# Kernel optimization log

Hardware: AMD Instinct MI355X
Metric: run time of the kernel (lower is better)

Reference implementation:

```python
import jax, jax.numpy as jnp
import numpy as np


def conv4d(x, w, b):
    """Valid 4D convolution.
    x: [B, Cin, T, D, H, W]; w: [Cout, Cin, kT, kD, kH, kW]; b: [Cout].
    Implemented as a fixed small loop over the kT kernel offsets, folding the
    output T positions into the batch of a 3D convolution (same math as the
    standard conv4d-via-conv3d decomposition used in torch).
    """
    B, Cin, T, D, H, W = x.shape
    Cout, _, kT, kD, kH, kW = w.shape
    To = T - kT + 1
    Do, Ho, Wo = D - kD + 1, H - kH + 1, W - kW + 1
    out = jnp.zeros((B * To, Cout, Do, Ho, Wo), dtype=x.dtype)
    for i in range(kT):  # kT in {3,4}: small fixed loop
        xs = jax.lax.slice_in_dim(x, i, i + To, axis=2)          # [B,Cin,To,D,H,W]
        xs = xs.transpose(0, 2, 1, 3, 4, 5).reshape(B * To, Cin, D, H, W)
        out = out + jax.lax.conv_general_dilated(
            xs, w[:, :, i], window_strides=(1, 1, 1), padding='VALID',
            dimension_numbers=('NCDHW', 'OIDHW', 'NCDHW'))
    out = out.reshape(B, To, Cout, Do, Ho, Wo).transpose(0, 2, 1, 3, 4, 5)
    return out + b[None, :, None, None, None, None]


def setup_inputs() -> dict:
    key = jax.random.key(0)
    ks = jax.random.split(key, 14)
    s = 0.1
    inp = {
        'x':  jax.random.normal(ks[0], (256, 1, 18, 18, 18, 18), dtype=jnp.float32),
        'w1': jax.random.normal(ks[1], (3, 1, 4, 4, 4, 4), dtype=jnp.float32) * s,
        'b1': jnp.zeros((3,), dtype=jnp.float32),
        'w2': jax.random.normal(ks[2], (3, 3, 4, 4, 4, 4), dtype=jnp.float32) * s,
        'b2': jnp.zeros((3,), dtype=jnp.float32),
        'w3': jax.random.normal(ks[3], (4, 3, 4, 4, 4, 4), dtype=jnp.float32) * s,
        'b3': jnp.zeros((4,), dtype=jnp.float32),
        'w4': jax.random.normal(ks[4], (5, 4, 4, 4, 4, 4), dtype=jnp.float32) * s,
        'b4': jnp.zeros((5,), dtype=jnp.float32),
        'w5': jax.random.normal(ks[5], (5, 5, 3, 3, 3, 3), dtype=jnp.float32) * s,
        'b5': jnp.zeros((5,), dtype=jnp.float32),
        'fc1_w': jax.random.normal(ks[6], (33, 1280), dtype=jnp.float32) * 0.02,
        'fc1_b': jnp.zeros((33,), dtype=jnp.float32),
        'fc2_w': jax.random.normal(ks[7], (1, 33), dtype=jnp.float32) * 0.02,
        'fc2_b': jnp.zeros((1,), dtype=jnp.float32),
    }
    return inp


def reference(x, w1, b1, w2, b2, w3, b3, w4, b4, w5, b5, fc1_w, fc1_b, fc2_w, fc2_b):
    h = jax.nn.relu(conv4d(x, w1, b1))
    h = jax.nn.relu(conv4d(h, w2, b2))
    h = jax.nn.relu(conv4d(h, w3, b3))
    h = jax.nn.relu(conv4d(h, w4, b4))
    h = jax.nn.relu(conv4d(h, w5, b5))   # [B, 5, 4, 4, 4, 4]
    h = h.reshape(h.shape[0], -1)        # [B, 1280]; Dropout is identity in eval
    h = jax.nn.relu(h @ fc1_w.T + fc1_b)
    return jax.nn.sigmoid(h @ fc2_w.T + fc2_b)  # [B, 1]
```

## Files before the change

kernel.cpp:

```cpp
#include <hip/hip_runtime.h>
#include <math.h>

#define BATCH 256
typedef unsigned int uint;
typedef unsigned short ushort;
typedef _Float16 half8 __attribute__((ext_vector_type(8)));
typedef float f32x4 __attribute__((ext_vector_type(4)));
typedef uint u32x4 __attribute__((ext_vector_type(4)));

#define GLOBAL_AS __attribute__((address_space(1)))
#define LDS_AS __attribute__((address_space(3)))

__device__ __forceinline__ ushort f2h(float f) {
  _Float16 h = (_Float16)f;
  return __builtin_bit_cast(ushort, h);
}
__device__ __forceinline__ float h2f(ushort u) {
  return (float)__builtin_bit_cast(_Float16, u);
}

template <int N>
__device__ __forceinline__ void waitv() {
  if constexpr (N == 0) {
    asm volatile("s_waitcnt vmcnt(0)" ::: "memory");
  } else if constexpr (N == 7) {
    asm volatile("s_waitcnt vmcnt(7)" ::: "memory");
  } else if constexpr (N == 9) {
    asm volatile("s_waitcnt vmcnt(9)" ::: "memory");
  } else if constexpr (N == 10) {
    asm volatile("s_waitcnt vmcnt(10)" ::: "memory");
  } else {
    static_assert(N == 0 || N == 7 || N == 9 || N == 10, "add literal");
  }
  __builtin_amdgcn_sched_barrier(0);
}

__global__ __launch_bounds__(256) void transpose_kernel(
    const float* __restrict__ x, uint* __restrict__ xt) {
  __shared__ uint tile[65][65];
  const int P = 104976, NPP = 52488;
  const int pp0 = blockIdx.x * 64, b0 = blockIdx.y * 64;
  const int tx = threadIdx.x & 63, ty = threadIdx.x >> 6;
  for (int r = 0; r < 64; r += 4) {
    const int bl = ty + r, pp = pp0 + tx;
    if (pp < NPP) {
      const float2 v = *(const float2*)(x + (size_t)(b0 + bl) * P + 2 * pp);
      tile[tx][bl] = (uint)f2h(v.x) | ((uint)f2h(v.y) << 16);
    }
  }
  if (threadIdx.x < 64 && pp0 + 64 < NPP) {
    const int bl = threadIdx.x;
    const float2 v =
        *(const float2*)(x + (size_t)(b0 + bl) * P + 2 * (pp0 + 64));
    tile[64][bl] = (uint)f2h(v.x) | ((uint)f2h(v.y) << 16);
  }
  __syncthreads();
  for (int r = ty; r < 64; r += 4) {
    const int pp = pp0 + r;
    if (pp >= NPP) break;
    const int wp = pp % 9, sh = pp / 9;
    if (wp & 1) continue;
    uint2 o;
    o.x = tile[r][tx];
    o.y = (wp == 8) ? 0u : tile[r + 1][tx];
    *(uint2*)(xt + (size_t)(sh * 5 + (wp >> 1)) * 512 + (b0 + tx) * 2) = o;
  }
}

template <int CIN, int COUT, int KK, int S>
__global__ __launch_bounds__(256) void build_b(
    const float* __restrict__ w, ushort* __restrict__ Bg) {
  const int chunk = blockIdx.x;
  const int kd = chunk % KK, kt = (chunk / KK) % KK, ci = chunk / (KK * KK);
  for (int e = threadIdx.x; e < 512; e += 256) {
    int n = e >> 5, k = e & 31;
    int kh = k >> 3, wi = k & 7;
    int co = n / S, dw = n % S;
    int kw = wi - dw;
    float v = 0.f;
    if (co < COUT && kh < KK && kw >= 0 && kw < KK)
      v = w[((((co * CIN + ci) * KK + kt) * KK + kd) * KK + kh) * KK + kw];
    Bg[chunk * 512 + n * 32 + k] = f2h(v);
  }
}

template <int CIN, int COUT, int KK, int TI, int GIN, int GOUT, int HB,
          int PADSTART, int PADEND>
__global__ __launch_bounds__(256) void conv_wave(
    const ushort* __restrict__ xin, const ushort* __restrict__ Bg,
    const float* __restrict__ bias, ushort* __restrict__ out) {
  constexpr int S = 4;
  constexpr int WO = TI - KK + 1;
  constexpr int HTILES = WO / HB;
  constexpr int NC = CIN * KK * KK;
  constexpr int RS = 4 + HB - 1;
  constexpr int CH = RS + 1;
  constexpr int sH = GIN * 1024, sD = TI * sH, sT = TI * sD, sC = TI * sT;
  constexpr int oH = GOUT * 1024, oD = WO * oH, oT = WO * oD, oC = WO * oT;

  __shared__ ushort slab[4][2][CH * 512];

  const int ht = blockIdx.x % HTILES;
  const int wt = blockIdx.x / HTILES;
  const int d = blockIdx.y, t = blockIdx.z;
  const int h0 = ht * HB, wb = wt * S;
  const int g0 = wb >> 2;

  const int tid = threadIdx.x;
  const int wave = tid >> 6, lane = tid & 63;
  const int quad = lane >> 4, mm = lane & 15;

  const int xsrc = (lane >> 5) * 1024 + wave * 256 + (lane & 31) * 8;
  const int bsrc = mm * 32 + quad * 8;

  f32x4 acc[HB][4];
#pragma unroll
  for (int dh = 0; dh < HB; dh++)
#pragma unroll
    for (int bt = 0; bt < 4; bt++) acc[dh][bt] = (f32x4){0.f, 0.f, 0.f, 0.f};

  auto stage = [&](int c, int buf) {
    const int kd = c % KK, kt2 = (c / KK) % KK, ci = c / (KK * KK);
    const ushort* base =
        xin + ci * sC + (t + kt2) * sT + (d + kd) * sD + h0 * sH + g0 * 1024;
    ushort* l = &slab[wave][buf][0];
#pragma unroll
    for (int r = 0; r < RS; r++)
      __builtin_amdgcn_global_load_lds(
          (const GLOBAL_AS uint*)(const void*)(base + r * sH + xsrc),
          (LDS_AS uint*)(void*)(l + r * 512), 16, 0, 0);
    __builtin_amdgcn_global_load_lds(
        (const GLOBAL_AS uint*)(const void*)(Bg + c * 512 + bsrc),
        (LDS_AS uint*)(void*)(l + RS * 512), 16, 0, 0);
  };

  stage(0, 0);

  for (int c = 0; c < NC; c++) {
    if (c + 1 < NC) {
      stage(c + 1, (c + 1) & 1);
      waitv<CH>();
    } else {
      waitv<0>();
    }
    const ushort* wsl = &slab[wave][c & 1][0];
    u32x4 traw = *(const u32x4*)(const void*)(wsl + RS * 512 + lane * 8);
    half8 tf = __builtin_bit_cast(half8, traw);
#pragma unroll
    for (int dh = 0; dh < HB; dh++) {
      const ushort* arow = wsl + (dh + quad) * 512;
#pragma unroll
      for (int bt = 0; bt < 4; bt++) {
        const int bb = bt * 16 + mm;
        uint2 lo = *(const uint2*)(const void*)(arow + bb * 4);
        uint2 hi = *(const uint2*)(const void*)(arow + 256 + bb * 4);
        half8 xf = __builtin_bit_cast(half8, (u32x4){lo.x, lo.y, hi.x, hi.y});
        acc[dh][bt] =
            __builtin_amdgcn_mfma_f32_16x16x32_f16(tf, xf, acc[dh][bt], 0, 0, 0);
      }
    }
  }

  const bool is_last = (wb + S >= WO);
  const int co = quad;
#pragma unroll
  for (int dh = 0; dh < HB; dh++)
#pragma unroll
    for (int bt = 0; bt < 4; bt++) {
      const int b = wave * 64 + bt * 16 + mm;
      ushort* obase = out + t * oT + d * oD + (h0 + dh) * oH + b * 4;
      f32x4 v = acc[dh][bt];
      if (co < COUT) {
        const float bv = bias[co];
        float r0 = (wb + 0 < WO) ? fmaxf(v[0] + bv, 0.f) : 0.f;
        float r1 = (wb + 1 < WO) ? fmaxf(v[1] + bv, 0.f) : 0.f;
        float r2 = (wb + 2 < WO) ? fmaxf(v[2] + bv, 0.f) : 0.f;
        float r3 = (wb + 3 < WO) ? fmaxf(v[3] + bv, 0.f) : 0.f;
        uint2 pk;
        pk.x = (uint)f2h(r0) | ((uint)f2h(r1) << 16);
        pk.y = (uint)f2h(r2) | ((uint)f2h(r3) << 16);
        *(uint2*)(void*)(obase + co * oC + g0 * 1024) = pk;
        if constexpr (PADEND > PADSTART) {
          if (is_last) {
#pragma unroll
            for (int w = PADSTART; w < PADEND; w += 2)
              *(uint*)(void*)(obase + co * oC + (w >> 2) * 1024 + (w & 3)) = 0u;
          }
        }
      }
    }
}

template <int CIN, int COUT, int KK, int TI, int GIN, int GOUT, int S, int HB,
          int PADSTART, int PADEND>
__global__ __launch_bounds__(256) void conv_mfma(
    const ushort* __restrict__ xin, const ushort* __restrict__ Bg,
    const float* __restrict__ bias, ushort* __restrict__ out) {
  constexpr int WO = TI - KK + 1;
  constexpr int HTILES = WO / HB;
  constexpr int NC = CIN * KK * KK;
  constexpr int RS = 4 + HB - 1;
  constexpr int GW = (S == 4 ? 2 : 3);
  constexpr int ROWU = GW * 1024;
  constexpr int PROW = GW * 2;
  constexpr int sH = GIN * 1024, sD = TI * sH, sT = TI * sD, sC = TI * sT;
  constexpr int oH = GOUT * 1024, oD = WO * oH, oT = WO * oD, oC = WO * oT;

  __shared__ ushort slab[2][RS * ROWU];

  const int ht = blockIdx.x % HTILES;
  const int wt = blockIdx.x / HTILES;
  const int d = blockIdx.y, t = blockIdx.z;
  const int h0 = ht * HB, wb = wt * S;
  const int g0 = wb >> 2;

  const int tid = threadIdx.x;
  const int wave = tid >> 6, lane = tid & 63;
  const int quad = lane >> 4, mm = lane & 15;

  f32x4 acc[HB][4];
#pragma unroll
  for (int dh = 0; dh < HB; dh++)
#pragma unroll
    for (int bt = 0; bt < 4; bt++) acc[dh][bt] = (f32x4){0.f, 0.f, 0.f, 0.f};

  auto stage = [&](int c, int buf) {
    const int kd = c % KK, kt2 = (c / KK) % KK, ci = c / (KK * KK);
    const ushort* base =
        xin + ci * sC + (t + kt2) * sT + (d + kd) * sD + g0 * 1024;
    for (int r = wave; r < RS; r += 4) {
      int row = h0 + r;
      if (row > TI - 1) row = TI - 1;
      const ushort* g = base + row * sH;
      ushort* l = &slab[buf][r * ROWU];
#pragma unroll
      for (int p = 0; p < PROW; p++) {
        __builtin_amdgcn_global_load_lds(
            (const GLOBAL_AS uint*)(const void*)(g + p * 512 + lane * 8),
            (LDS_AS uint*)(void*)(l + p * 512), 16, 0, 0);
      }
    }
  };

  stage(0, 0);

  for (int c = 0; c < NC; c++) {
    __syncthreads();
    if (c + 1 < NC) stage(c + 1, (c + 1) & 1);

    u32x4 traw = *(const u32x4*)(const void*)(Bg + c * 512 + mm * 32 + quad * 8);
    half8 tf = __builtin_bit_cast(half8, traw);
    const int buf = c & 1;

#pragma unroll
    for (int dh = 0; dh < HB; dh++) {
      const ushort* arow = &slab[buf][(dh + quad) * ROWU];
#pragma unroll
      for (int bt = 0; bt < 4; bt++) {
        const int bidx = ((wave * 4 + bt) * 16 + mm) * 4;
        u32x4 raw;
        if ((wb & 2) == 0) {
          uint2 lo = *(const uint2*)(const void*)(arow + bidx);
          uint2 hi = *(const uint2*)(const void*)(arow + 1024 + bidx);
          raw = (u32x4){lo.x, lo.y, hi.x, hi.y};
        } else {
          uint c0 = *(const uint*)(const void*)(arow + bidx + 2);
          uint2 md = *(const uint2*)(const void*)(arow + 1024 + bidx);
          uint c1 = *(const uint*)(const void*)(arow + 2048 + bidx);
          raw = (u32x4){c0, md.x, md.y, c1};
        }
        half8 xf = __builtin_bit_cast(half8, raw);
        acc[dh][bt] =
            __builtin_amdgcn_mfma_f32_16x16x32_f16(tf, xf, acc[dh][bt], 0, 0, 0);
      }
    }
  }

  const bool is_last = (wb + S >= WO);
#pragma unroll
  for (int dh = 0; dh < HB; dh++)
#pragma unroll
    for (int bt = 0; bt < 4; bt++) {
      const int b = (wave * 4 + bt) * 16 + mm;
      ushort* obase = out + t * oT + d * oD + (h0 + dh) * oH + b * 4;
      f32x4 v = acc[dh][bt];
      const int co0 = quad * 2, co1 = co0 + 1;
      if (co0 < COUT) {
        const float bv = bias[co0];
        float r0 = fmaxf(v[0] + bv, 0.f), r1 = fmaxf(v[1] + bv, 0.f);
        *(uint*)(void*)(obase + co0 * oC + g0 * 1024 + (wb & 3)) =
            (uint)f2h(r0) | ((uint)f2h(r1) << 16);
      }
      if (co1 < COUT) {
        const float bv = bias[co1];
        float r2 = fmaxf(v[2] + bv, 0.f), r3 = fmaxf(v[3] + bv, 0.f);
        *(uint*)(void*)(obase + co1 * oC + g0 * 1024 + (wb & 3)) =
            (uint)f2h(r2) | ((uint)f2h(r3) << 16);
      }
      if constexpr (PADEND > PADSTART) {
        if (is_last) {
#pragma unroll
          for (int cc = 0; cc < 2; cc++) {
            const int co = quad * 2 + cc;
            if (co < COUT) {
#pragma unroll
              for (int w = PADSTART; w < PADEND; w += 2)
                *(uint*)(void*)(obase + co * oC + (w >> 2) * 1024 + (w & 3)) =
                    0u;
            }
          }
        }
      }
    }
}

__global__ __launch_bounds__(256) void fc1_kernel(
    const ushort* __restrict__ h, const float* __restrict__ w,
    const float* __restrict__ bias, float* __restrict__ out) {
  const int o = blockIdx.x, b = threadIdx.x;
  const float* wr = w + o * 1280;
  float a0 = 0.f, a1 = 0.f, a2 = 0.f, a3 = 0.f;
#pragma unroll 4
  for (int kq = 0; kq < 320; kq++) {
    const uint2 hv = *(const uint2*)(const void*)(h + (kq * 256 + b) * 4);
    a0 = fmaf(h2f((ushort)(hv.x & 0xffffu)), wr[4 * kq + 0], a0);
    a1 = fmaf(h2f((ushort)(hv.x >> 16)), wr[4 * kq + 1], a1);
    a2 = fmaf(h2f((ushort)(hv.y & 0xffffu)), wr[4 * kq + 2], a2);
    a3 = fmaf(h2f((ushort)(hv.y >> 16)), wr[4 * kq + 3], a3);
  }
  float acc = (a0 + a1) + (a2 + a3) + bias[o];
  out[o * BATCH + b] = acc > 0.f ? acc : 0.f;
}

__global__ __launch_bounds__(256) void fc2_kernel(
    const float* __restrict__ r, const float* __restrict__ w,
    const float* __restrict__ bias, float* __restrict__ out) {
  const int b = threadIdx.x;
  float acc = bias[0];
#pragma unroll
  for (int o = 0; o < 33; o++) acc = fmaf(r[o * BATCH + b], w[o], acc);
  out[b] = 1.f / (1.f + expf(-acc));
}

extern "C" void kernel_launch(void* const* d_in, const int* in_sizes, int n_in,
                              void* d_out, int out_size, void* d_ws,
                              size_t ws_size, hipStream_t stream) {
  const float* x    = (const float*)d_in[0];
  const float* w1   = (const float*)d_in[1];
  const float* b1   = (const float*)d_in[2];
  const float* w2   = (const float*)d_in[3];
  const float* b2   = (const float*)d_in[4];
  const float* w3   = (const float*)d_in[5];
  const float* b3   = (const float*)d_in[6];
  const float* w4   = (const float*)d_in[7];
  const float* b4   = (const float*)d_in[8];
  const float* w5   = (const float*)d_in[9];
  const float* b5   = (const float*)d_in[10];
  const float* fc1w = (const float*)d_in[11];
  const float* fc1b = (const float*)d_in[12];
  const float* fc2w = (const float*)d_in[13];
  const float* fc2b = (const float*)d_in[14];
  float* out = (float*)d_out;

  ushort* wsu = (ushort*)d_ws;
  ushort* R0 = wsu;
  ushort* R1 = wsu + 29900000;
  ushort* Bgb = wsu + 71400000;
  float* fo = (float*)(wsu + 71520000);

  ushort* xt = R0;
  ushort* h1 = R1;
  ushort* h2 = R0;
  ushort* h3 = R1;
  ushort* h4 = R0;
  ushort* h5 = R1;

  ushort* B1 = Bgb;
  ushort* B2 = Bgb + 16 * 512;
  ushort* B3 = Bgb + 64 * 512;
  ushort* B4 = Bgb + 112 * 512;
  ushort* B5 = Bgb + 176 * 512;

  build_b<1, 3, 4, 4><<<16, 256, 0, stream>>>(w1, B1);
  build_b<3, 3, 4, 4><<<48, 256, 0, stream>>>(w2, B2);
  build_b<3, 4, 4, 4><<<48, 256, 0, stream>>>(w3, B3);
  build_b<4, 5, 4, 2><<<64, 256, 0, stream>>>(w4, B4);
  build_b<5, 5, 3, 2><<<45, 256, 0, stream>>>(w5, B5);

  transpose_kernel<<<dim3(821, 4), 256, 0, stream>>>(x, (uint*)xt);

  conv_wave<1, 3, 4, 18, 5, 4, 5, 0, 0>
      <<<dim3(12, 15, 15), 256, 0, stream>>>(xt, B1, b1, h1);
  conv_wave<3, 3, 4, 15, 4, 4, 6, 12, 16>
      <<<dim3(6, 12, 12), 256, 0, stream>>>(h1, B2, b2, h2);
  conv_wave<3, 4, 4, 12, 4, 3, 3, 0, 0>
      <<<dim3(9, 9, 9), 256, 0, stream>>>(h2, B3, b3, h3);

  conv_mfma<4, 5, 4, 9, 3, 3, 2, 2, 6, 12>
      <<<dim3(9, 6, 6), 256, 0, stream>>>(h3, B4, b4, h4);
  conv_mfma<5, 5, 3, 6, 3, 1, 2, 2, 0, 0>
      <<<dim3(4, 4, 4), 256, 0, stream>>>(h4, B5, b5, h5);

  fc1_kernel<<<33, 256, 0, stream>>>(h5, fc1w, fc1b, fo);
  fc2_kernel<<<1, 256, 0, stream>>>(fo, fc2w, fc2b, out);
}
```

Before: 721.6 us.

## Swizzle conv_wave blocks across XCDs and load weight fragments directly to registers

The 3D grid of conv_wave becomes a 1D launch, with block ids remapped so that consecutive tiles land on the same XCD. Neighbouring tiles share input rows, so this is meant to improve L2 reuse. The per-chunk weight fragment is now read straight from global memory into registers instead of being staged through LDS, which shrinks each LDS slab. The chunk loop is unrolled by two with fixed double-buffer indices, and the vmcnt waits count the register weight load. This adds a requirement that the chunk count be even, and weight-load latency is now exposed in registers rather than hidden by the LDS copy.

```diff
diff --git a/kernel.cpp b/kernel.cpp
--- a/kernel.cpp
+++ b/kernel.cpp
@@ -33,6 +33,13 @@
     static_assert(N == 0 || N == 7 || N == 9 || N == 10, "add literal");
   }
   __builtin_amdgcn_sched_barrier(0);
+}
+
+template <int NWG>
+__device__ __forceinline__ int xcd_swz(int bid) {
+  constexpr int Q = NWG / 8, R = NWG % 8;
+  const int x = bid & 7, i = bid >> 3;
+  return (x < R ? x * (Q + 1) : R * (Q + 1) + (x - R) * Q) + i;
 }
 
 __global__ __launch_bounds__(256) void transpose_kernel(
@@ -92,17 +99,23 @@
   constexpr int S = 4;
   constexpr int WO = TI - KK + 1;
   constexpr int HTILES = WO / HB;
+  constexpr int WTILES = (WO + S - 1) / S;
+  constexpr int GX = HTILES * WTILES;
+  constexpr int NWG = GX * WO * WO;
   constexpr int NC = CIN * KK * KK;
+  static_assert(NC % 2 == 0, "pair-unrolled chunk loop needs even NC");
   constexpr int RS = 4 + HB - 1;
   constexpr int CH = RS + 1;
   constexpr int sH = GIN * 1024, sD = TI * sH, sT = TI * sD, sC = TI * sT;
   constexpr int oH = GOUT * 1024, oD = WO * oH, oT = WO * oD, oC = WO * oT;
 
-  __shared__ ushort slab[4][2][CH * 512];
-
-  const int ht = blockIdx.x % HTILES;
-  const int wt = blockIdx.x / HTILES;
-  const int d = blockIdx.y, t = blockIdx.z;
+  __shared__ ushort slab[4][2][RS * 512];
+
+  const int wg = xcd_swz<NWG>(blockIdx.x);
+  const int xb = wg % GX;
+  const int d = (wg / GX) % WO;
+  const int t = wg / (GX * WO);
+  const int ht = xb % HTILES, wt = xb / HTILES;
   const int h0 = ht * HB, wb = wt * S;
   const int g0 = wb >> 2;
 
@@ -129,23 +142,15 @@
       __builtin_amdgcn_global_load_lds(
           (const GLOBAL_AS uint*)(const void*)(base + r * sH + xsrc),
           (LDS_AS uint*)(void*)(l + r * 512), 16, 0, 0);
-    __builtin_amdgcn_global_load_lds(
-        (const GLOBAL_AS uint*)(const void*)(Bg + c * 512 + bsrc),
-        (LDS_AS uint*)(void*)(l + RS * 512), 16, 0, 0);
   };
 
-  stage(0, 0);
-
-  for (int c = 0; c < NC; c++) {
-    if (c + 1 < NC) {
-      stage(c + 1, (c + 1) & 1);
-      waitv<CH>();
-    } else {
-      waitv<0>();
-    }
-    const ushort* wsl = &slab[wave][c & 1][0];
-    u32x4 traw = *(const u32x4*)(const void*)(wsl + RS * 512 + lane * 8);
+  auto load_tf = [&](int c) -> u32x4 {
+    return *(const u32x4*)(const void*)(Bg + c * 512 + bsrc);
+  };
+
+  auto compute = [&](int buf, u32x4 traw) {
     half8 tf = __builtin_bit_cast(half8, traw);
+    const ushort* wsl = &slab[wave][buf][0];
 #pragma unroll
     for (int dh = 0; dh < HB; dh++) {
       const ushort* arow = wsl + (dh + quad) * 512;
@@ -159,6 +164,27 @@
             __builtin_amdgcn_mfma_f32_16x16x32_f16(tf, xf, acc[dh][bt], 0, 0, 0);
       }
     }
+  };
+
+  stage(0, 0);
+  u32x4 tfA = load_tf(0);
+  u32x4 tfB;
+
+  for (int c = 0; c < NC; c += 2) {
+    tfB = load_tf(c + 1);
+    stage(c + 1, 1);
+    waitv<CH>();
+    compute(0, tfA);
+    __builtin_amdgcn_sched_barrier(0);
+    if (c + 2 < NC) {
+      tfA = load_tf(c + 2);
+      stage(c + 2, 0);
+      waitv<CH>();
+    } else {
+      waitv<0>();
+    }
+    compute(1, tfB);
+    __builtin_amdgcn_sched_barrier(0);
   }
 
   const bool is_last = (wb + S >= WO);
@@ -390,11 +416,11 @@
   transpose_kernel<<<dim3(821, 4), 256, 0, stream>>>(x, (uint*)xt);
 
   conv_wave<1, 3, 4, 18, 5, 4, 5, 0, 0>
-      <<<dim3(12, 15, 15), 256, 0, stream>>>(xt, B1, b1, h1);
+      <<<2700, 256, 0, stream>>>(xt, B1, b1, h1);
   conv_wave<3, 3, 4, 15, 4, 4, 6, 12, 16>
-      <<<dim3(6, 12, 12), 256, 0, stream>>>(h1, B2, b2, h2);
+      <<<864, 256, 0, stream>>>(h1, B2, b2, h2);
   conv_wave<3, 4, 4, 12, 4, 3, 3, 0, 0>
-      <<<dim3(9, 9, 9), 256, 0, stream>>>(h2, B3, b3, h3);
+      <<<729, 256, 0, stream>>>(h2, B3, b3, h3);
 
   conv_mfma<4, 5, 4, 9, 3, 3, 2, 2, 6, 12>
       <<<dim3(9, 6, 6), 256, 0, stream>>>(h3, B4, b4, h4);
```

Result: faster. 657.0 us (-9.0%).
